# Kernel optimization log

Hardware: AMD Instinct MI355X
Metric: run time of the kernel (lower is better)

## Reference

```python
import jax, jax.numpy as jnp
import numpy as np

B, S, D, H, L, V, DFF = 8, 1024, 256, 8, 4, 100, 1024
EPS = 1e-5


def _pos_encodings(seq_len, d):
    # Faithful to SinusoidalPositionalEmbedding (NOTE: original uses sin for both halves)
    pos = jnp.arange(seq_len, dtype=jnp.float32)[:, None]        # [S,1]
    freqs = jnp.arange(d, dtype=jnp.float32)[None, :]            # [1,D]
    sin_even = jnp.sin(pos / 10000.0 ** (freqs[:, 0::2] / d))    # [S,D/2]
    sin_odd = jnp.sin(pos / 10000.0 ** (freqs[:, 1::2] / d))     # [S,D/2]
    return jnp.concatenate([sin_even, sin_odd], axis=1)          # [S,D]


def _self_attention_mask(sequence_length, seq_len):
    # create_self_attention_mask with causal=True; assumes max(sequence_length)==seq_len
    r = jnp.arange(seq_len)[None, :]                             # [1,S]
    m = (r < sequence_length[:, None]).astype(jnp.float32)       # [B,S]
    m = m[:, :, None] * m[:, None, :]                            # [B,S,S]
    causal = jnp.tril(jnp.ones((seq_len, seq_len), jnp.float32))
    return m * causal                                            # [B,S,S]


def setup_inputs() -> dict:
    key = jax.random.key(0)
    ks = jax.random.split(key, 20)
    n = lambda k, shape, s=0.02: (jax.random.normal(k, shape) * s).astype(jnp.float32)
    return {
        "output_ids": jax.random.randint(ks[0], (B, S), 0, V),
        "target_sequence_length": jnp.full((B,), S, dtype=jnp.int32),
        "embedding": n(ks[1], (V, D), 1.0),
        "Wq": n(ks[2], (L, D, D)), "bq": jnp.zeros((L, D), jnp.float32),
        "Wk": n(ks[3], (L, D, D)), "bk": jnp.zeros((L, D), jnp.float32),
        "Wv": n(ks[4], (L, D, D)), "bv": jnp.zeros((L, D), jnp.float32),
        "Wo": n(ks[5], (L, D, D)), "bo": jnp.zeros((L, D), jnp.float32),
        "W1": n(ks[6], (L, D, DFF)), "b1": jnp.zeros((L, DFF), jnp.float32),
        "W2": n(ks[7], (L, DFF, D)), "b2": jnp.zeros((L, D), jnp.float32),
        "g1": jnp.ones((L, D), jnp.float32), "be1": jnp.zeros((L, D), jnp.float32),
        "g2": jnp.ones((L, D), jnp.float32), "be2": jnp.zeros((L, D), jnp.float32),
        "Wc": n(ks[8], (D, V)), "bc": jnp.zeros((V,), jnp.float32),
    }


def _forward(output_ids, target_sequence_length, embedding, Wq, bq, Wk, bk, Wv, bv,
             Wo, bo, W1, b1, W2, b2, g1, be1, g2, be2, Wc, bc):
    Bn, Sn = output_ids.shape
    d = embedding.shape[1]
    x = embedding[output_ids] + _pos_encodings(Sn, d)[None]      # [B,S,D]
    mask = _self_attention_mask(target_sequence_length, Sn)[:, None] > 0  # [B,1,S,S] bool

    def ln(h, g, b):
        m = h.mean(-1, keepdims=True)
        v = jnp.var(h, axis=-1, keepdims=True)
        return (h - m) / jnp.sqrt(v + EPS) * g + b

    def step(x, p):
        wq, bq_, wk, bk_, wv, bv_, wo, bo_, w1, b1_, w2, b2_, g1_, be1_, g2_, be2_ = p
        q = (x @ wq + bq_).reshape(Bn, Sn, H, -1)
        k = (x @ wk + bk_).reshape(Bn, Sn, H, -1)
        v = (x @ wv + bv_).reshape(Bn, Sn, H, -1)
        dh = q.shape[-1]
        scores = jnp.einsum('bqhd,bkhd->bhqk', q, k) / jnp.sqrt(jnp.float32(dh))
        attn = jax.nn.softmax(jnp.where(mask, scores, -1e9), axis=-1)
        attn = jnp.where(mask, attn, 0.0)                        # post-softmax mask (as original)
        y = jnp.einsum('bhqk,bkhd->bqhd', attn, v).reshape(Bn, Sn, -1)
        y = y @ wo + bo_
        x = ln(x + y, g1_, be1_)
        ff = jax.nn.relu(x @ w1 + b1_) @ w2 + b2_
        x = ln(x + ff, g2_, be2_)
        return x, None

    x, _ = jax.lax.scan(step, x, (Wq, bq, Wk, bk, Wv, bv, Wo, bo, W1, b1, W2, b2, g1, be1, g2, be2))
    return x @ Wc + bc                                           # logits [B,S,V]


def reference(output_ids, target_sequence_length, embedding, Wq, bq, Wk, bk, Wv, bv,
              Wo, bo, W1, b1, W2, b2, g1, be1, g2, be2, Wc, bc):
    return _forward(output_ids, target_sequence_length, embedding, Wq, bq, Wk, bk, Wv, bv,
                    Wo, bo, W1, b1, W2, b2, g1, be1, g2, be2, Wc, bc)
```

## Files before the change

kernel.cpp:

```cpp
#include <hip/hip_runtime.h>
#include <hip/hip_bf16.h>
#include <stdint.h>

#define B_   8
#define S_   1024
#define D_   256
#define H_   8
#define DH_  32
#define L_   4
#define V_   100
#define DFF_ 1024
#define M_   (B_*S_)

using bf16 = __hip_bfloat16;
typedef __bf16 bf16x8 __attribute__((ext_vector_type(8)));
typedef float  f32x4  __attribute__((ext_vector_type(4)));

static __device__ __forceinline__ float b2f(unsigned short u) {
  union { unsigned int i; float f; } w; w.i = ((unsigned int)u) << 16; return w.f;
}

static __device__ __forceinline__ void load_lds16(const void* g, void* l) {
  __builtin_amdgcn_global_load_lds((const __attribute__((address_space(1))) void*)g,
                                   (__attribute__((address_space(3))) void*)l,
                                   16, 0, 0);
}

template<int CTRL>
static __device__ __forceinline__ float dppf(float v) {
  union { float f; int i; } a, r;
  a.f = v;
  r.i = __builtin_amdgcn_update_dpp(0, a.i, CTRL, 0xF, 0xF, true);
  return r.f;
}
static __device__ __forceinline__ float red_max16(float v) {
  v = fmaxf(v, dppf<0xB1>(v));
  v = fmaxf(v, dppf<0x4E>(v));
  v = fmaxf(v, dppf<0x141>(v));
  v = fmaxf(v, dppf<0x140>(v));
  return v;
}
static __device__ __forceinline__ float red_sum16(float v) {
  v += dppf<0xB1>(v);
  v += dppf<0x4E>(v);
  v += dppf<0x141>(v);
  v += dppf<0x140>(v);
  return v;
}

__global__ void prep_t(const float* __restrict__ Wq, const float* __restrict__ Wk,
                       const float* __restrict__ Wv, const float* __restrict__ Wo,
                       const float* __restrict__ W1, const float* __restrict__ W2,
                       const float* __restrict__ Wc,
                       const float* __restrict__ bq, const float* __restrict__ bk,
                       const float* __restrict__ bv,
                       bf16* __restrict__ WqkvT, bf16* __restrict__ WoT,
                       bf16* __restrict__ W1T, bf16* __restrict__ W2T,
                       bf16* __restrict__ WcT, float* __restrict__ bqkv)
{
  const int z = blockIdx.z;
  if (z == 25) {
    if (blockIdx.x || blockIdx.y) return;
    const int tid = threadIdx.y*32 + threadIdx.x;
    for (int i = tid; i < L_*768; i += 256) {
      const int l2 = i / 768, j = i % 768;
      const float* src = (j < 256) ? bq : (j < 512) ? bk : bv;
      bqkv[i] = src[l2*256 + (j & 255)];
    }
    return;
  }
  const float* src; bf16* dst; int R, C, Cd;
  if (z < 12) {
    const int l = z / 3, w = z % 3;
    src = ((w == 0) ? Wq : (w == 1) ? Wk : Wv) + (size_t)l*65536;
    R = 256; C = 256; Cd = 256;
    dst = WqkvT + (size_t)l*196608 + (size_t)w*65536;
  } else if (z < 16) {
    const int l = z - 12;
    src = Wo + (size_t)l*65536; R = 256; C = 256; Cd = 256;
    dst = WoT + (size_t)l*65536;
  } else if (z < 20) {
    const int l = z - 16;
    src = W1 + (size_t)l*262144; R = 256; C = 1024; Cd = 1024;
    dst = W1T + (size_t)l*262144;
  } else if (z < 24) {
    const int l = z - 20;
    src = W2 + (size_t)l*262144; R = 1024; C = 256; Cd = 256;
    dst = W2T + (size_t)l*262144;
  } else {
    src = Wc; R = 256; C = 100; Cd = 128;
    dst = WcT;
  }
  const int c0 = blockIdx.x*32, r0 = blockIdx.y*32;
  if (c0 >= Cd || r0 >= R) return;
  __shared__ float t[32][33];
  #pragma unroll
  for (int i = 0; i < 4; ++i) {
    const int r = r0 + threadIdx.y + i*8;
    const int c = c0 + threadIdx.x;
    t[threadIdx.y + i*8][threadIdx.x] = (r < R && c < C) ? src[(size_t)r*C + c] : 0.f;
  }
  __syncthreads();
  #pragma unroll
  for (int i = 0; i < 4; ++i) {
    const int c = c0 + threadIdx.y + i*8;
    const int r = r0 + threadIdx.x;
    if (c < Cd && r < R)
      dst[(size_t)c*R + r] = (bf16)t[threadIdx.x][threadIdx.y + i*8];
  }
}

__global__ void embed_kernel(const int* __restrict__ ids, const float* __restrict__ emb,
                             bf16* __restrict__ x)
{
  const int bs = blockIdx.x;
  const int d  = threadIdx.x;
  const int s  = bs & (S_-1);
  const int id = ids[bs];
  const int f  = (d < 128) ? (2*d) : (2*(d-128)+1);
  const float inv = powf(10000.f, -(float)f * (1.f/256.f));
  const float pe  = sinf((float)s * inv);
  x[(size_t)bs*D_ + d] = (bf16)(emb[(size_t)id*D_ + d] + pe);
}

__global__ __launch_bounds__(256) void gemm_qkv(
    const bf16* __restrict__ A, const bf16* __restrict__ BT,
    const float* __restrict__ bias,
    bf16* __restrict__ qp, bf16* __restrict__ kp, bf16* __restrict__ vt)
{
  __shared__ bf16 As[128*32];
  __shared__ bf16 Bs[64*32];
  __shared__ bf16 Vs[64][136];
  const int tid  = threadIdx.x;
  const int lane = tid & 63, wave = tid >> 6;
  const int quad = lane >> 4, l15 = lane & 15;
  const int m0 = blockIdx.x * 128;
  const int n0 = blockIdx.y * 64;
  const int wm = (wave & 1) * 64;
  const int wn = (wave >> 1) * 32;
  const int K = 256;

  const bf16* a0 = A  + (size_t)m0 * K;
  const bf16* b0 = BT + (size_t)n0 * K;
  const int row = tid >> 2;
  const int ch  = (tid & 3) * 8;

  f32x4 acc[4][2] = {};

  for (int k0 = 0; k0 < K; k0 += 32) {
    __syncthreads();
    load_lds16(a0 + (size_t)row*K      + k0 + ch, (char*)As + (size_t)wave*1024);
    load_lds16(a0 + (size_t)(row+64)*K + k0 + ch, (char*)As + 4096 + (size_t)wave*1024);
    load_lds16(b0 + (size_t)row*K      + k0 + ch, (char*)Bs + (size_t)wave*1024);
    __syncthreads();
    bf16x8 af[4], bfr[2];
    #pragma unroll
    for (int mt = 0; mt < 4; ++mt)
      af[mt] = *(const bf16x8*)(As + (wm + mt*16 + l15)*32 + quad*8);
    #pragma unroll
    for (int nt = 0; nt < 2; ++nt)
      bfr[nt] = *(const bf16x8*)(Bs + (wn + nt*16 + l15)*32 + quad*8);
    #pragma unroll
    for (int mt = 0; mt < 4; ++mt)
      #pragma unroll
      for (int nt = 0; nt < 2; ++nt)
        acc[mt][nt] = __builtin_amdgcn_mfma_f32_16x16x32_bf16(af[mt], bfr[nt], acc[mt][nt], 0, 0, 0);
  }

  const int seg = n0 >> 8;
  const int b  = m0 >> 10;
  const int s0 = m0 & 1023;

  if (seg < 2) {
    bf16* dst = seg ? kp : qp;
    #pragma unroll
    for (int nt = 0; nt < 2; ++nt) {
      const int n  = n0 + wn + nt*16 + l15;
      const int nn = n & 255;
      const int h = nn >> 5, d = nn & 31;
      const float bvs = bias[n];
      bf16* hb = dst + (((size_t)b*H_ + h)*S_)*DH_ + d;
      #pragma unroll
      for (int mt = 0; mt < 4; ++mt) {
        const int ml = wm + mt*16 + quad*4;
        #pragma unroll
        for (int r = 0; r < 4; ++r)
          hb[(size_t)(s0 + ml + r)*DH_] = (bf16)(acc[mt][nt][r] + bvs);
      }
    }
  } else {
    #pragma unroll
    for (int nt = 0; nt < 2; ++nt) {
      const int nl = wn + nt*16 + l15;
      const float bvs = bias[n0 + nl];
      #pragma unroll
      for (int mt = 0; mt < 4; ++mt) {
        const int ml = wm + mt*16 + quad*4;
        #pragma unroll
        for (int r = 0; r < 4; ++r)
          Vs[nl][ml + r] = (bf16)(acc[mt][nt][r] + bvs);
      }
    }
    __syncthreads();
    #pragma unroll
    for (int t = 0; t < 2; ++t) {
      const int vrow = (tid >> 3) + 32*t;
      const int soff = (tid & 7) * 16;
      const int nn = (n0 + vrow) & 255;
      const int h = nn >> 5, d = nn & 31;
      bf16* dst = vt + (((size_t)b*H_ + h)*DH_ + d)*S_ + s0 + soff;
      *(bf16x8*)dst       = *(const bf16x8*)&Vs[vrow][soff];
      *(bf16x8*)(dst + 8) = *(const bf16x8*)&Vs[vrow][soff + 8];
    }
  }
}

template<bool RELU, bool OUT_BF16>
__global__ __launch_bounds__(256) void gemm_bt(
    const bf16* __restrict__ A, const bf16* __restrict__ BT,
    const float* __restrict__ bias, void* __restrict__ C,
    int M, int N, int K)
{
  __shared__ bf16 As[128*32];
  __shared__ bf16 Bs[64*32];
  const int tid  = threadIdx.x;
  const int lane = tid & 63, wave = tid >> 6;
  const int quad = lane >> 4, l15 = lane & 15;
  const int m0 = blockIdx.x * 128;
  const int n0 = blockIdx.y * 64;
  const int wm = (wave & 1) * 64;
  const int wn = (wave >> 1) * 32;

  const bf16* a0 = A  + (size_t)m0 * K;
  const bf16* b0 = BT + (size_t)n0 * K;
  const int row = tid >> 2;
  const int ch  = (tid & 3) * 8;

  f32x4 acc[4][2] = {};

  for (int k0 = 0; k0 < K; k0 += 32) {
    __syncthreads();
    load_lds16(a0 + (size_t)row*K      + k0 + ch, (char*)As + (size_t)wave*1024);
    load_lds16(a0 + (size_t)(row+64)*K + k0 + ch, (char*)As + 4096 + (size_t)wave*1024);
    load_lds16(b0 + (size_t)row*K      + k0 + ch, (char*)Bs + (size_t)wave*1024);
    __syncthreads();
    bf16x8 af[4], bfr[2];
    #pragma unroll
    for (int mt = 0; mt < 4; ++mt)
      af[mt] = *(const bf16x8*)(As + (wm + mt*16 + l15)*32 + quad*8);
    #pragma unroll
    for (int nt = 0; nt < 2; ++nt)
      bfr[nt] = *(const bf16x8*)(Bs + (wn + nt*16 + l15)*32 + quad*8);
    #pragma unroll
    for (int mt = 0; mt < 4; ++mt)
      #pragma unroll
      for (int nt = 0; nt < 2; ++nt)
        acc[mt][nt] = __builtin_amdgcn_mfma_f32_16x16x32_bf16(af[mt], bfr[nt], acc[mt][nt], 0, 0, 0);
  }

  #pragma unroll
  for (int nt = 0; nt < 2; ++nt) {
    const int n = n0 + wn + nt*16 + l15;
    const float bvs = bias[n];
    #pragma unroll
    for (int mt = 0; mt < 4; ++mt) {
      const int mr = m0 + wm + mt*16 + quad*4;
      #pragma unroll
      for (int r = 0; r < 4; ++r) {
        float v = acc[mt][nt][r] + bvs;
        if (RELU) v = fmaxf(v, 0.f);
        if (OUT_BF16) ((bf16*)C)[(size_t)(mr + r)*N + n] = (bf16)v;
        else          ((float*)C)[(size_t)(mr + r)*N + n] = v;
      }
    }
  }
}

template<bool RELU, bool OUT_BF16, bool NMASK>
__global__ __launch_bounds__(256) void gemm_bt64(
    const bf16* __restrict__ A, const bf16* __restrict__ BT,
    const float* __restrict__ bias, void* __restrict__ C,
    int M, int N, int K)
{
  __shared__ bf16 As[64*32];
  __shared__ bf16 Bs[64*32];
  const int tid  = threadIdx.x;
  const int lane = tid & 63, wave = tid >> 6;
  const int quad = lane >> 4, l15 = lane & 15;
  const int m0 = blockIdx.x * 64;
  const int n0 = blockIdx.y * 64;
  const int wm = (wave & 1) * 32;
  const int wn = (wave >> 1) * 32;

  const bf16* a0 = A  + (size_t)m0 * K;
  const bf16* b0 = BT + (size_t)n0 * K;
  const int row = tid >> 2;
  const int ch  = (tid & 3) * 8;

  f32x4 acc[2][2] = {};

  for (int k0 = 0; k0 < K; k0 += 32) {
    __syncthreads();
    load_lds16(a0 + (size_t)row*K + k0 + ch, (char*)As + (size_t)wave*1024);
    load_lds16(b0 + (size_t)row*K + k0 + ch, (char*)Bs + (size_t)wave*1024);
    __syncthreads();
    bf16x8 af[2], bfr[2];
    #pragma unroll
    for (int mt = 0; mt < 2; ++mt)
      af[mt] = *(const bf16x8*)(As + (wm + mt*16 + l15)*32 + quad*8);
    #pragma unroll
    for (int nt = 0; nt < 2; ++nt)
      bfr[nt] = *(const bf16x8*)(Bs + (wn + nt*16 + l15)*32 + quad*8);
    #pragma unroll
    for (int mt = 0; mt < 2; ++mt)
      #pragma unroll
      for (int nt = 0; nt < 2; ++nt)
        acc[mt][nt] = __builtin_amdgcn_mfma_f32_16x16x32_bf16(af[mt], bfr[nt], acc[mt][nt], 0, 0, 0);
  }

  #pragma unroll
  for (int nt = 0; nt < 2; ++nt) {
    const int n = n0 + wn + nt*16 + l15;
    if (NMASK && n >= N) continue;
    const float bvs = bias[n];
    #pragma unroll
    for (int mt = 0; mt < 2; ++mt) {
      const int mr = m0 + wm + mt*16 + quad*4;
      #pragma unroll
      for (int r = 0; r < 4; ++r) {
        float v = acc[mt][nt][r] + bvs;
        if (RELU) v = fmaxf(v, 0.f);
        if (OUT_BF16) ((bf16*)C)[(size_t)(mr + r)*N + n] = (bf16)v;
        else          ((float*)C)[(size_t)(mr + r)*N + n] = v;
      }
    }
  }
}

__global__ __launch_bounds__(256) void attn_kernel(
    const bf16* __restrict__ qp, const bf16* __restrict__ kp,
    const bf16* __restrict__ vt, const int* __restrict__ tsl,
    bf16* __restrict__ out)
{
  const int h = blockIdx.y, b = blockIdx.z;
  const int lane = threadIdx.x & 63, wave = threadIdx.x >> 6;
  const int quad = lane >> 4, l15 = lane & 15;
  const int sid = blockIdx.x + wave*16;
  const int q0 = sid*16;
  const int len = tsl[b];

  __shared__ bf16 Pl[4][16*64];

  const size_t bh = (size_t)b*H_ + h;
  const bf16* qb = qp + bh*S_*DH_;
  const bf16* kb = kp + bh*S_*DH_;
  const bf16* vb = vt + bh*DH_*S_;

  const bf16x8 qf = *(const bf16x8*)(qb + (size_t)(q0 + l15)*DH_ + quad*8);

  const float NEG = -1e30f;
  float m_run[4], l_run[4], al[4];
  f32x4 o0 = {0.f,0.f,0.f,0.f}, o1 = {0.f,0.f,0.f,0.f};
  #pragma unroll
  for (int r = 0; r < 4; ++r) { m_run[r] = NEG; l_run[r] = 0.f; }

  const float scale = 0.17677669529663687f;
  bf16* pw = &Pl[wave][0];
  const int qrow0 = q0 + quad*4;

  if (len >= S_) {
    const int dt = sid >> 2;
    for (int ks = 0; ks <= dt; ++ks) {
      const int k0 = ks*64;
      f32x4 s[4];
      #pragma unroll
      for (int nt = 0; nt < 4; ++nt) {
        const bf16x8 kf = *(const bf16x8*)(kb + (size_t)(k0 + nt*16 + l15)*DH_ + quad*8);
        const f32x4 z = {0.f,0.f,0.f,0.f};
        s[nt] = __builtin_amdgcn_mfma_f32_16x16x32_bf16(qf, kf, z, 0, 0, 0);
      }
      float mx[4];
      if (ks == dt) {
        #pragma unroll
        for (int r = 0; r < 4; ++r) mx[r] = NEG;
        #pragma unroll
        for (int nt = 0; nt < 4; ++nt) {
          const int kpos = k0 + nt*16 + l15;
          #pragma unroll
          for (int r = 0; r < 4; ++r) {
            const float v = (kpos <= qrow0 + r) ? s[nt][r] * scale : NEG;
            s[nt][r] = v;
            mx[r] = fmaxf(mx[r], v);
          }
        }
      } else {
        #pragma unroll
        for (int r = 0; r < 4; ++r) {
          float v0 = s[0][r] * scale; s[0][r] = v0;
          float v1 = s[1][r] * scale; s[1][r] = v1;
          float v2 = s[2][r] * scale; s[2][r] = v2;
          float v3 = s[3][r] * scale; s[3][r] = v3;
          mx[r] = fmaxf(fmaxf(v0, v1), fmaxf(v2, v3));
        }
      }
      #pragma unroll
      for (int r = 0; r < 4; ++r) {
        const float mn = fmaxf(m_run[r], red_max16(mx[r]));
        al[r] = __expf(m_run[r] - mn);
        m_run[r] = mn;
      }
      float ls[4];
      #pragma unroll
      for (int r = 0; r < 4; ++r) {
        float p0 = __expf(s[0][r] - m_run[r]); s[0][r] = p0;
        float p1 = __expf(s[1][r] - m_run[r]); s[1][r] = p1;
        float p2 = __expf(s[2][r] - m_run[r]); s[2][r] = p2;
        float p3 = __expf(s[3][r] - m_run[r]); s[3][r] = p3;
        ls[r] = (p0 + p1) + (p2 + p3);
      }
      #pragma unroll
      for (int r = 0; r < 4; ++r) {
        l_run[r] = l_run[r]*al[r] + red_sum16(ls[r]);
        o0[r] *= al[r];
        o1[r] *= al[r];
      }
      #pragma unroll
      for (int nt = 0; nt < 4; ++nt)
        #pragma unroll
        for (int r = 0; r < 4; ++r)
          pw[(quad*4+r)*64 + nt*16 + l15] = (bf16)s[nt][r];
      asm volatile("s_waitcnt lgkmcnt(0)" ::: "memory");
      #pragma unroll
      for (int kc = 0; kc < 2; ++kc) {
        const bf16x8 pf = *(const bf16x8*)(pw + l15*64 + kc*32 + quad*8);
        const bf16x8 vf0 = *(const bf16x8*)(vb + (size_t)l15*S_ + k0 + kc*32 + quad*8);
        o0 = __builtin_amdgcn_mfma_f32_16x16x32_bf16(pf, vf0, o0, 0, 0, 0);
        const bf16x8 vf1 = *(const bf16x8*)(vb + (size_t)(16 + l15)*S_ + k0 + kc*32 + quad*8);
        o1 = __builtin_amdgcn_mfma_f32_16x16x32_bf16(pf, vf1, o1, 0, 0, 0);
      }
    }
  } else {
    const int nk = (sid >> 2) + 1;
    for (int ks = 0; ks < nk; ++ks) {
      const int k0 = ks*64;
      f32x4 s[4];
      #pragma unroll
      for (int nt = 0; nt < 4; ++nt) {
        const bf16x8 kf = *(const bf16x8*)(kb + (size_t)(k0 + nt*16 + l15)*DH_ + quad*8);
        const f32x4 z = {0.f,0.f,0.f,0.f};
        s[nt] = __builtin_amdgcn_mfma_f32_16x16x32_bf16(qf, kf, z, 0, 0, 0);
      }
      float mx[4];
      #pragma unroll
      for (int r = 0; r < 4; ++r) mx[r] = NEG;
      #pragma unroll
      for (int nt = 0; nt < 4; ++nt) {
        const int kpos = k0 + nt*16 + l15;
        #pragma unroll
        for (int r = 0; r < 4; ++r) {
          const int qr = qrow0 + r;
          const bool ok = (kpos <= qr) && (kpos < len) && (qr < len);
          const float v = ok ? s[nt][r] * scale : NEG;
          s[nt][r] = v;
          mx[r] = fmaxf(mx[r], v);
        }
      }
      #pragma unroll
      for (int r = 0; r < 4; ++r) {
        const float mn = fmaxf(m_run[r], red_max16(mx[r]));
        al[r] = (m_run[r] > -1e29f) ? __expf(m_run[r] - mn) : 0.f;
        m_run[r] = mn;
      }
      float ls[4] = {0.f,0.f,0.f,0.f};
      #pragma unroll
      for (int nt = 0; nt < 4; ++nt)
        #pragma unroll
        for (int r = 0; r < 4; ++r) {
          const float vv = s[nt][r];
          const float p = (vv > -1e29f && m_run[r] > -1e29f) ? __expf(vv - m_run[r]) : 0.f;
          s[nt][r] = p;
          ls[r] += p;
        }
      #pragma unroll
      for (int r = 0; r < 4; ++r) {
        l_run[r] = l_run[r]*al[r] + red_sum16(ls[r]);
        o0[r] *= al[r];
        o1[r] *= al[r];
      }
      #pragma unroll
      for (int nt = 0; nt < 4; ++nt)
        #pragma unroll
        for (int r = 0; r < 4; ++r)
          pw[(quad*4+r)*64 + nt*16 + l15] = (bf16)s[nt][r];
      asm volatile("s_waitcnt lgkmcnt(0)" ::: "memory");
      #pragma unroll
      for (int kc = 0; kc < 2; ++kc) {
        const bf16x8 pf = *(const bf16x8*)(pw + l15*64 + kc*32 + quad*8);
        const bf16x8 vf0 = *(const bf16x8*)(vb + (size_t)l15*S_ + k0 + kc*32 + quad*8);
        o0 = __builtin_amdgcn_mfma_f32_16x16x32_bf16(pf, vf0, o0, 0, 0, 0);
        const bf16x8 vf1 = *(const bf16x8*)(vb + (size_t)(16 + l15)*S_ + k0 + kc*32 + quad*8);
        o1 = __builtin_amdgcn_mfma_f32_16x16x32_bf16(pf, vf1, o1, 0, 0, 0);
      }
    }
  }

  bf16* ob = out + (size_t)b*S_*D_ + h*DH_;
  #pragma unroll
  for (int r = 0; r < 4; ++r) {
    const float inv = 1.f / fmaxf(l_run[r], 1e-30f);
    const size_t rowoff = (size_t)(q0 + quad*4 + r)*D_;
    ob[rowoff + l15]      = (bf16)(o0[r]*inv);
    ob[rowoff + 16 + l15] = (bf16)(o1[r]*inv);
  }
}

__global__ void addln_kernel(const bf16* x, const float* y,
                             const float* g, const float* be, bf16* xo)
{
  const int row  = blockIdx.x*4 + (threadIdx.x >> 6);
  const int lane = threadIdx.x & 63;
  const bf16*  xr = x + (size_t)row*D_ + lane*4;
  const float* yr = y + (size_t)row*D_ + lane*4;
  const ushort4 xs = *(const ushort4*)xr;
  const float4  yv = *(const float4*)yr;
  const float v0 = b2f(xs.x) + yv.x;
  const float v1 = b2f(xs.y) + yv.y;
  const float v2 = b2f(xs.z) + yv.z;
  const float v3 = b2f(xs.w) + yv.w;
  float sm = v0+v1+v2+v3;
  #pragma unroll
  for (int off = 1; off < 64; off <<= 1) sm += __shfl_xor(sm, off);
  const float mean = sm * (1.f/256.f);
  const float d0 = v0-mean, d1 = v1-mean, d2 = v2-mean, d3 = v3-mean;
  float qs = d0*d0 + d1*d1 + d2*d2 + d3*d3;
  #pragma unroll
  for (int off = 1; off < 64; off <<= 1) qs += __shfl_xor(qs, off);
  const float inv = rsqrtf(qs*(1.f/256.f) + 1e-5f);
  const float4 gv = *(const float4*)(g + lane*4);
  const float4 bv = *(const float4*)(be + lane*4);
  bf16 o0 = (bf16)(d0*inv*gv.x + bv.x);
  bf16 o1 = (bf16)(d1*inv*gv.y + bv.y);
  bf16 o2 = (bf16)(d2*inv*gv.z + bv.z);
  bf16 o3 = (bf16)(d3*inv*gv.w + bv.w);
  ushort4 ov = { *(unsigned short*)&o0, *(unsigned short*)&o1,
                 *(unsigned short*)&o2, *(unsigned short*)&o3 };
  *(ushort4*)(xo + (size_t)row*D_ + lane*4) = ov;
}

extern "C" void kernel_launch(void* const* d_in, const int* in_sizes, int n_in,
                              void* d_out, int out_size, void* d_ws, size_t ws_size,
                              hipStream_t stream)
{
  const int*   ids = (const int*)d_in[0];
  const int*   tsl = (const int*)d_in[1];
  const float* emb = (const float*)d_in[2];
  const float* Wq  = (const float*)d_in[3];
  const float* bq  = (const float*)d_in[4];
  const float* Wk  = (const float*)d_in[5];
  const float* bk  = (const float*)d_in[6];
  const float* Wv  = (const float*)d_in[7];
  const float* bv  = (const float*)d_in[8];
  const float* Wo  = (const float*)d_in[9];
  const float* bo  = (const float*)d_in[10];
  const float* W1  = (const float*)d_in[11];
  const float* b1  = (const float*)d_in[12];
  const float* W2  = (const float*)d_in[13];
  const float* b2  = (const float*)d_in[14];
  const float* g1  = (const float*)d_in[15];
  const float* be1 = (const float*)d_in[16];
  const float* g2  = (const float*)d_in[17];
  const float* be2 = (const float*)d_in[18];
  const float* Wc  = (const float*)d_in[19];
  const float* bc  = (const float*)d_in[20];

  if (ws_size < (size_t)40*1024*1024) return;

  char* p = (char*)d_ws;
  auto carve = [&](size_t bytes) { void* r = (void*)p; p += (bytes + 255) & ~(size_t)255; return r; };
  bf16*  x     = (bf16*) carve((size_t)M_*D_*2);
  char*  big   = (char*) carve((size_t)M_*DFF_*2);
  char*  pkbuf = (char*) carve((size_t)12*1024*1024);
  bf16*  WqkvT = (bf16*) carve((size_t)L_*768*256*2);
  bf16*  WoT   = (bf16*) carve((size_t)L_*65536*2);
  bf16*  W1T   = (bf16*) carve((size_t)L_*262144*2);
  bf16*  W2T   = (bf16*) carve((size_t)L_*262144*2);
  bf16*  WcT   = (bf16*) carve((size_t)128*256*2);
  float* bqkv  = (float*)carve((size_t)L_*768*4);

  bf16*  aout = (bf16*)big;
  bf16*  ff1  = (bf16*)big;
  bf16*  qp   = (bf16*)pkbuf;
  bf16*  kp   = (bf16*)(pkbuf + (size_t)4*1024*1024);
  bf16*  vt   = (bf16*)(pkbuf + (size_t)8*1024*1024);
  float* yf   = (float*)pkbuf;

  prep_t<<<dim3(32,32,26), dim3(32,8), 0, stream>>>(Wq,Wk,Wv,Wo,W1,W2,Wc,bq,bk,bv,
                                                    WqkvT,WoT,W1T,W2T,WcT,bqkv);
  embed_kernel<<<dim3(M_), 256, 0, stream>>>(ids, emb, x);

  for (int l = 0; l < L_; ++l) {
    gemm_qkv<<<dim3(64,12), 256, 0, stream>>>(
        x, WqkvT + (size_t)l*768*256, bqkv + l*768, qp, kp, vt);
    attn_kernel<<<dim3(16,8,8), 256, 0, stream>>>(qp, kp, vt, tsl, aout);
    gemm_bt64<false,false,false><<<dim3(128,4), 256, 0, stream>>>(
        aout, WoT + (size_t)l*65536, bo + l*256, yf, M_, 256, 256);
    addln_kernel<<<dim3(2048), 256, 0, stream>>>(x, yf, g1 + l*256, be1 + l*256, x);
    gemm_bt<true,true><<<dim3(64,16), 256, 0, stream>>>(
        x, W1T + (size_t)l*262144, b1 + l*1024, ff1, M_, 1024, 256);
    gemm_bt64<false,false,false><<<dim3(128,4), 256, 0, stream>>>(
        ff1, W2T + (size_t)l*262144, b2 + l*256, yf, M_, 256, 1024);
    addln_kernel<<<dim3(2048), 256, 0, stream>>>(x, yf, g2 + l*256, be2 + l*256, x);
  }

  gemm_bt64<false,false,true><<<dim3(128,2), 256, 0, stream>>>(
      x, WcT, bc, (float*)d_out, M_, V_, 256);
}
```

Baseline: 485.7 us.

## Fuse output-projection and FFN-down GEMMs with residual add and LayerNorm

Adds a gemm_ln kernel that computes a 16-row by full-256-column GEMM tile per block, then adds bias and the residual and applies LayerNorm in the epilogue. It uses cross-wave sums through shared memory and writes bf16 x in place. This replaces the gemm_bt64 plus addln_kernel pairs, removing the fp32 intermediate round-trip and two launches per layer. The cost is a small M tile of 16 rows, so each block reloads the whole 256xK weight panel with no double buffering. It also uses a one-pass E[x^2]-mean^2 variance, which is less numerically stable.

```diff
diff --git a/kernel.cpp b/kernel.cpp
--- a/kernel.cpp
+++ b/kernel.cpp
@@ -337,6 +337,105 @@
   }
 }
 
+__global__ __launch_bounds__(256) void gemm_ln(
+    const bf16* __restrict__ A, const bf16* __restrict__ BT,
+    const float* __restrict__ bias, const float* __restrict__ g,
+    const float* __restrict__ be, bf16* xio, int K)
+{
+  __shared__ bf16 As[16*32];
+  __shared__ bf16 Bs[256*32];
+  __shared__ bf16 Xs[16][264];
+  __shared__ float sums[4][16][2];
+
+  const int tid  = threadIdx.x;
+  const int lane = tid & 63, wave = tid >> 6;
+  const int quad = lane >> 4, l15 = lane & 15;
+  const int m0 = blockIdx.x * 16;
+  const int wn = wave * 64;
+
+  const bf16* a0 = A + (size_t)m0 * K;
+  const int ch = (tid & 3) * 8;
+
+  f32x4 acc[4] = {};
+
+  for (int k0 = 0; k0 < K; k0 += 32) {
+    __syncthreads();
+    if (wave == 0)
+      load_lds16(a0 + (size_t)(lane >> 2)*K + k0 + (lane & 3)*8, (char*)As);
+    #pragma unroll
+    for (int j = 0; j < 4; ++j)
+      load_lds16(BT + (size_t)(64*j + (tid >> 2))*K + k0 + ch,
+                 (char*)Bs + j*4096 + (size_t)wave*1024);
+    __syncthreads();
+    const bf16x8 af = *(const bf16x8*)(As + l15*32 + quad*8);
+    #pragma unroll
+    for (int nt = 0; nt < 4; ++nt) {
+      const bf16x8 bfr = *(const bf16x8*)(Bs + (wn + nt*16 + l15)*32 + quad*8);
+      acc[nt] = __builtin_amdgcn_mfma_f32_16x16x32_bf16(af, bfr, acc[nt], 0, 0, 0);
+    }
+  }
+
+  {
+    const int xr = tid >> 4, xc = (tid & 15) * 16;
+    const bf16* src = xio + (size_t)(m0 + xr)*D_ + xc;
+    *(bf16x8*)&Xs[xr][xc]     = *(const bf16x8*)src;
+    *(bf16x8*)&Xs[xr][xc + 8] = *(const bf16x8*)(src + 8);
+  }
+  __syncthreads();
+
+  float v[4][4];
+  float bvs[4];
+  #pragma unroll
+  for (int nt = 0; nt < 4; ++nt) bvs[nt] = bias[wn + nt*16 + l15];
+  #pragma unroll
+  for (int r = 0; r < 4; ++r) {
+    const int rr = quad*4 + r;
+    float ls = 0.f, lq = 0.f;
+    #pragma unroll
+    for (int nt = 0; nt < 4; ++nt) {
+      const float y = acc[nt][r] + bvs[nt];
+      const float xv = b2f(*(const unsigned short*)&Xs[rr][wn + nt*16 + l15]);
+      const float vv = xv + y;
+      v[r][nt] = vv;
+      ls += vv;
+      lq += vv*vv;
+    }
+    ls = red_sum16(ls);
+    lq = red_sum16(lq);
+    if (l15 == 0) { sums[wave][rr][0] = ls; sums[wave][rr][1] = lq; }
+  }
+  __syncthreads();
+
+  float gv[4], bev[4];
+  #pragma unroll
+  for (int nt = 0; nt < 4; ++nt) {
+    gv[nt]  = g[wn + nt*16 + l15];
+    bev[nt] = be[wn + nt*16 + l15];
+  }
+  #pragma unroll
+  for (int r = 0; r < 4; ++r) {
+    const int rr = quad*4 + r;
+    const float ts = sums[0][rr][0] + sums[1][rr][0] + sums[2][rr][0] + sums[3][rr][0];
+    const float tq = sums[0][rr][1] + sums[1][rr][1] + sums[2][rr][1] + sums[3][rr][1];
+    const float mean = ts * (1.f/256.f);
+    const float var  = tq * (1.f/256.f) - mean*mean;
+    const float inv  = rsqrtf(var + 1e-5f);
+    #pragma unroll
+    for (int nt = 0; nt < 4; ++nt) {
+      const bf16 o = (bf16)((v[r][nt] - mean)*inv*gv[nt] + bev[nt]);
+      Xs[rr][wn + nt*16 + l15] = o;
+    }
+  }
+  __syncthreads();
+
+  {
+    const int xr = tid >> 4, xc = (tid & 15) * 16;
+    bf16* dst = xio + (size_t)(m0 + xr)*D_ + xc;
+    *(bf16x8*)dst       = *(const bf16x8*)&Xs[xr][xc];
+    *(bf16x8*)(dst + 8) = *(const bf16x8*)&Xs[xr][xc + 8];
+  }
+}
+
 __global__ __launch_bounds__(256) void attn_kernel(
     const bf16* __restrict__ qp, const bf16* __restrict__ kp,
     const bf16* __restrict__ vt, const int* __restrict__ tsl,
@@ -512,39 +611,6 @@
     ob[rowoff + l15]      = (bf16)(o0[r]*inv);
     ob[rowoff + 16 + l15] = (bf16)(o1[r]*inv);
   }
-}
-
-__global__ void addln_kernel(const bf16* x, const float* y,
-                             const float* g, const float* be, bf16* xo)
-{
-  const int row  = blockIdx.x*4 + (threadIdx.x >> 6);
-  const int lane = threadIdx.x & 63;
-  const bf16*  xr = x + (size_t)row*D_ + lane*4;
-  const float* yr = y + (size_t)row*D_ + lane*4;
-  const ushort4 xs = *(const ushort4*)xr;
-  const float4  yv = *(const float4*)yr;
-  const float v0 = b2f(xs.x) + yv.x;
-  const float v1 = b2f(xs.y) + yv.y;
-  const float v2 = b2f(xs.z) + yv.z;
-  const float v3 = b2f(xs.w) + yv.w;
-  float sm = v0+v1+v2+v3;
-  #pragma unroll
-  for (int off = 1; off < 64; off <<= 1) sm += __shfl_xor(sm, off);
-  const float mean = sm * (1.f/256.f);
-  const float d0 = v0-mean, d1 = v1-mean, d2 = v2-mean, d3 = v3-mean;
-  float qs = d0*d0 + d1*d1 + d2*d2 + d3*d3;
-  #pragma unroll
-  for (int off = 1; off < 64; off <<= 1) qs += __shfl_xor(qs, off);
-  const float inv = rsqrtf(qs*(1.f/256.f) + 1e-5f);
-  const float4 gv = *(const float4*)(g + lane*4);
-  const float4 bv = *(const float4*)(be + lane*4);
-  bf16 o0 = (bf16)(d0*inv*gv.x + bv.x);
-  bf16 o1 = (bf16)(d1*inv*gv.y + bv.y);
-  bf16 o2 = (bf16)(d2*inv*gv.z + bv.z);
-  bf16 o3 = (bf16)(d3*inv*gv.w + bv.w);
-  ushort4 ov = { *(unsigned short*)&o0, *(unsigned short*)&o1,
-                 *(unsigned short*)&o2, *(unsigned short*)&o3 };
-  *(ushort4*)(xo + (size_t)row*D_ + lane*4) = ov;
 }
 
 extern "C" void kernel_launch(void* const* d_in, const int* in_sizes, int n_in,
@@ -592,7 +658,6 @@
   bf16*  qp   = (bf16*)pkbuf;
   bf16*  kp   = (bf16*)(pkbuf + (size_t)4*1024*1024);
   bf16*  vt   = (bf16*)(pkbuf + (size_t)8*1024*1024);
-  float* yf   = (float*)pkbuf;
 
   prep_t<<<dim3(32,32,26), dim3(32,8), 0, stream>>>(Wq,Wk,Wv,Wo,W1,W2,Wc,bq,bk,bv,
                                                     WqkvT,WoT,W1T,W2T,WcT,bqkv);
@@ -602,14 +667,12 @@
     gemm_qkv<<<dim3(64,12), 256, 0, stream>>>(
         x, WqkvT + (size_t)l*768*256, bqkv + l*768, qp, kp, vt);
     attn_kernel<<<dim3(16,8,8), 256, 0, stream>>>(qp, kp, vt, tsl, aout);
-    gemm_bt64<false,false,false><<<dim3(128,4), 256, 0, stream>>>(
-        aout, WoT + (size_t)l*65536, bo + l*256, yf, M_, 256, 256);
-    addln_kernel<<<dim3(2048), 256, 0, stream>>>(x, yf, g1 + l*256, be1 + l*256, x);
+    gemm_ln<<<dim3(512), 256, 0, stream>>>(
+        aout, WoT + (size_t)l*65536, bo + l*256, g1 + l*256, be1 + l*256, x, 256);
     gemm_bt<true,true><<<dim3(64,16), 256, 0, stream>>>(
         x, W1T + (size_t)l*262144, b1 + l*1024, ff1, M_, 1024, 256);
-    gemm_bt64<false,false,false><<<dim3(128,4), 256, 0, stream>>>(
-        ff1, W2T + (size_t)l*262144, b2 + l*256, yf, M_, 256, 1024);
-    addln_kernel<<<dim3(2048), 256, 0, stream>>>(x, yf, g2 + l*256, be2 + l*256, x);
+    gemm_ln<<<dim3(512), 256, 0, stream>>>(
+        ff1, W2T + (size_t)l*262144, b2 + l*256, g2 + l*256, be2 + l*256, x, 1024);
   }
 
   gemm_bt64<false,false,true><<<dim3(128,2), 256, 0, stream>>>(
```

Result: no change. 481.9 us (-0.8%).
